# Optimization experiments

Hardware: AMD Instinct MI355X
Metric: run time of the kernel (lower is better)

Reference implementation:

```python
import jax, jax.numpy as jnp
import numpy as np

B, S, LD, Hh, Ww = 64, 32, 16, 32, 18
D, NH, HD, FF, L = 512, 8, 64, 2048, 6
IN = LD * Hh * Ww  # 9216
EPS = 1e-5


def setup_inputs() -> dict:
    key = jax.random.key(0)
    ks = jax.random.split(key, 8)
    p = lambda k, s: jax.random.normal(k, s, jnp.float32) * 0.02
    return {
        "x": jax.random.normal(ks[0], (B, S, LD, Hh, Ww), jnp.float32),
        "inp_w": p(ks[1], (D, IN)), "inp_b": jnp.zeros((D,), jnp.float32),
        "in_proj_w": p(ks[2], (L, 3 * D, D)), "in_proj_b": jnp.zeros((L, 3 * D), jnp.float32),
        "out_w": p(ks[3], (L, D, D)), "out_b": jnp.zeros((L, D), jnp.float32),
        "ln1_w": jnp.ones((L, D), jnp.float32), "ln1_b": jnp.zeros((L, D), jnp.float32),
        "ln2_w": jnp.ones((L, D), jnp.float32), "ln2_b": jnp.zeros((L, D), jnp.float32),
        "ff1_w": p(ks[4], (L, FF, D)), "ff1_b": jnp.zeros((L, FF), jnp.float32),
        "ff2_w": p(ks[5], (L, D, FF)), "ff2_b": jnp.zeros((L, D), jnp.float32),
        "outp_w": p(ks[6], (IN, D)), "outp_b": jnp.zeros((IN,), jnp.float32),
    }


def _layernorm(x, w, b):
    mu = jnp.mean(x, -1, keepdims=True)
    var = jnp.mean(jnp.square(x - mu), -1, keepdims=True)
    return (x - mu) * jax.lax.rsqrt(var + EPS) * w + b


def _rope(x, cos, sin):
    # x: [B,S,NH,HD]; torchtune interleaved-pair rotation, rope applied BEFORE qk projection
    x2 = x.reshape(*x.shape[:-1], HD // 2, 2)
    x0, x1 = x2[..., 0], x2[..., 1]
    c = cos[None, :, None, :]
    s = sin[None, :, None, :]
    out = jnp.stack([x0 * c - x1 * s, x1 * c + x0 * s], axis=-1)
    return out.reshape(x.shape)


def reference(x, inp_w, inp_b, in_proj_w, in_proj_b, out_w, out_b,
              ln1_w, ln1_b, ln2_w, ln2_b, ff1_w, ff1_b, ff2_w, ff2_b,
              outp_w, outp_b):
    b, s = x.shape[0], x.shape[1]
    h = x.reshape(b, s, IN) @ inp_w.T + inp_b  # [B,S,D]

    theta = 1.0 / (10000.0 ** (jnp.arange(0, HD, 2, dtype=jnp.float32) / HD))
    ang = jnp.arange(s, dtype=jnp.float32)[:, None] * theta  # [S, HD/2]
    cos, sin = jnp.cos(ang), jnp.sin(ang)
    mask = jnp.triu(jnp.full((s, s), -jnp.inf, jnp.float32), k=1)  # causal additive mask
    scale = 1.0 / np.sqrt(HD)

    for i in range(L):
        # RoPE on full hidden state (pre-projection), used for q and k; v uses unrotated h
        hr = _rope(h.reshape(b, s, NH, HD), cos, sin).reshape(b, s, D)
        wq, wk, wv = in_proj_w[i, :D], in_proj_w[i, D:2 * D], in_proj_w[i, 2 * D:]
        bq, bk, bv = in_proj_b[i, :D], in_proj_b[i, D:2 * D], in_proj_b[i, 2 * D:]
        q = (hr @ wq.T + bq).reshape(b, s, NH, HD)
        k = (hr @ wk.T + bk).reshape(b, s, NH, HD)
        v = (h @ wv.T + bv).reshape(b, s, NH, HD)
        scores = jnp.einsum('bqhd,bkhd->bhqk', q, k) * scale + mask
        attn = jax.nn.softmax(scores, axis=-1)
        ctx = jnp.einsum('bhqk,bkhd->bqhd', attn, v).reshape(b, s, D)
        sa = ctx @ out_w[i].T + out_b[i]
        h = _layernorm(h + sa, ln1_w[i], ln1_b[i])  # post-norm (norm_first=False)
        ff = jax.nn.gelu(h @ ff1_w[i].T + ff1_b[i], approximate=False) @ ff2_w[i].T + ff2_b[i]
        h = _layernorm(h + ff, ln2_w[i], ln2_b[i])

    out = h @ outp_w.T + outp_b
    return out.reshape(b, s, LD, Hh, Ww)
```

## Files before the change

### kernel.cpp

```cpp
#include <hip/hip_runtime.h>
#include <hip/hip_bf16.h>
#include <math.h>


typedef __attribute__((ext_vector_type(8))) short bf16x8;
typedef __attribute__((ext_vector_type(4))) short bf16x4;
typedef __attribute__((ext_vector_type(8))) float f32x8;
typedef __attribute__((ext_vector_type(4))) float f32x4;

#define LN_EPS 1e-5f

__device__ inline float bf2f(__hip_bfloat16 v) { return __bfloat162float(v); }
__device__ inline __hip_bfloat16 f2bf(float f) { return __float2bfloat16(f); }

__device__ __forceinline__ void gload_lds16(const __hip_bfloat16* g, __hip_bfloat16* l) {
    __builtin_amdgcn_global_load_lds(
        (const __attribute__((address_space(1))) unsigned*)g,
        (__attribute__((address_space(3))) unsigned*)l, 16, 0, 0);
}

__device__ __forceinline__ void sync_tile() {
    asm volatile("s_waitcnt vmcnt(0) lgkmcnt(0)" ::: "memory");
    __builtin_amdgcn_s_barrier();
    asm volatile("" ::: "memory");
}

__global__ __launch_bounds__(1024) void rope_prep(float* __restrict__ tab) {
    const int t = threadIdx.x;
    const int s = t >> 5, p = t & 31;
    const float theta = powf(10000.f, -(float)p / 32.f);
    float sn, cs;
    sincosf((float)s * theta, &sn, &cs);
    tab[t * 2] = cs;
    tab[t * 2 + 1] = sn;
}

struct CvtSeg { const float* src; __hip_bfloat16* dst; };
struct CvtArgs { CvtSeg seg[16]; long cum[17]; };

__global__ __launch_bounds__(256) void convert_all(CvtArgs a, long total8) {
    for (long i = (long)blockIdx.x * 256 + threadIdx.x; i < total8;
         i += (long)gridDim.x * 256) {
        int s = 0;
        while (i >= a.cum[s + 1]) ++s;
        const long off = i - a.cum[s];
        const f32x8 x = *((const f32x8*)a.seg[s].src + off);
        union { bf16x8 v; __hip_bfloat16 b[8]; } o;
#pragma unroll
        for (int t = 0; t < 8; ++t) o.b[t] = f2bf(x[t]);
        *((bf16x8*)a.seg[s].dst + off) = o.v;
    }
}

template<int BM, int BN, int EPI, int OUT, int AMODE, int SWZ>
__global__ __launch_bounds__(256) void gemm_bt(
    const void* __restrict__ Araw, int bn_split,
    const float* __restrict__ rtab,
    const __hip_bfloat16* __restrict__ W,
    const __hip_bfloat16* __restrict__ bias,
    void* __restrict__ Cv,
    int M, int N, int Ktot, int KC)
{
    constexpr int FM = BM / 32, FN = BN / 32;
    constexpr int CPT_A = BM / 32, CPT_B = BN / 32;
    __shared__ __align__(16) __hip_bfloat16 sA[BM * 64];
    __shared__ __align__(16) __hip_bfloat16 sB[BN * 64];

    const int tid = threadIdx.x, lane = tid & 63, wave = tid >> 6;
    const int wr = wave >> 1, wc = wave & 1;
    const int lr = lane & 15, lk = lane >> 4;

    int bm, bn, zz;
    if (SWZ == 0) {
        const int nbm = gridDim.x, nbn = gridDim.y;
        const int nwg = nbm * nbn;
        const int orig = blockIdx.y * nbm + blockIdx.x;
        const int q8 = nwg >> 3, r8 = nwg & 7;
        const int xcd = orig & 7, loc = orig >> 3;
        const int f = (xcd < r8 ? xcd * (q8 + 1) : r8 * (q8 + 1) + (xcd - r8) * q8) + loc;
        bm = f % nbm; bn = f / nbm; zz = blockIdx.z;
    } else {
        const int bid = blockIdx.x;
        const int xcd = bid & 7, loc = bid >> 3;
        const int nbn = N / BN;
        const int per = (gridDim.x >> 3) / nbn;
        bn = loc % nbn;
        const int gid = xcd * per + loc / nbn;
        bm = gid % (M / BM); zz = gid / (M / BM);
    }
    const int kbeg = zz * KC, kend = kbeg + KC;
    const bool dorot = (AMODE == 2) && (bn < bn_split);

    const __hip_bfloat16* Ab = (const __hip_bfloat16*)Araw + (long)bm * BM * Ktot;
    const float*          Af = (const float*)Araw + (long)bm * BM * Ktot;
    const __hip_bfloat16* Wb = W + (long)bn * BN * Ktot;

    f32x4 acc[FM][FN];
#pragma unroll
    for (int i = 0; i < FM; ++i)
#pragma unroll
        for (int j = 0; j < FN; ++j) acc[i][j] = (f32x4){0.f, 0.f, 0.f, 0.f};

    f32x8  aregf[CPT_A];
    bf16x8 aregb[CPT_A];
    f32x8  csreg[CPT_A];

    auto stageA_g = [&](int k0) {
#pragma unroll
        for (int c = 0; c < CPT_A; ++c) {
            const int ch = tid + c * 256, row = ch >> 3, co = ch & 7;
            gload_lds16(&Ab[(long)row * Ktot + k0 + ((co ^ (row & 7)) * 8)],
                        (__hip_bfloat16*)((char*)sA + ch * 16));
        }
    };
    auto stageB_g = [&](int k0) {
#pragma unroll
        for (int c = 0; c < CPT_B; ++c) {
            const int ch = tid + c * 256, row = ch >> 3, co = ch & 7;
            gload_lds16(&Wb[(long)row * Ktot + k0 + ((co ^ (row & 7)) * 8)],
                        (__hip_bfloat16*)((char*)sB + ch * 16));
        }
    };
    auto issueA = [&](int k0) {
#pragma unroll
        for (int c = 0; c < CPT_A; ++c) {
            const int ch = tid + c * 256, row = ch >> 3, co = ch & 7;
            if (AMODE == 1) aregf[c] = *(const f32x8*)&Af[(long)row * Ktot + k0 + co * 8];
            if (AMODE == 2) {
                aregb[c] = *(const bf16x8*)&Ab[(long)row * Ktot + k0 + co * 8];
                if (dorot)
                    csreg[c] = *(const f32x8*)&rtab[((bm * BM + row) & 31) * 64 + co * 8];
            }
        }
    };
    auto writeA = [&]() {
#pragma unroll
        for (int c = 0; c < CPT_A; ++c) {
            const int ch = tid + c * 256, row = ch >> 3, co = ch & 7;
            union { bf16x8 v; __hip_bfloat16 b[8]; } t;
            if (AMODE == 1) {
#pragma unroll
                for (int j = 0; j < 8; ++j) t.b[j] = f2bf(aregf[c][j]);
            } else {
                t.v = aregb[c];
                if (dorot) {
#pragma unroll
                    for (int qd = 0; qd < 4; ++qd) {
                        const float c_ = csreg[c][qd * 2], sn = csreg[c][qd * 2 + 1];
                        const float x0 = bf2f(t.b[2 * qd]);
                        const float x1 = bf2f(t.b[2 * qd + 1]);
                        t.b[2 * qd]     = f2bf(x0 * c_ - x1 * sn);
                        t.b[2 * qd + 1] = f2bf(x1 * c_ + x0 * sn);
                    }
                }
            }
            *(bf16x8*)((char*)sA + row * 128 + ((co ^ (row & 7)) << 4)) = t.v;
        }
    };
    auto compute = [&]() {
        bf16x8 af[2][FM], bfr[2][FN];
#pragma unroll
        for (int ks = 0; ks < 2; ++ks) {
#pragma unroll
            for (int i = 0; i < FM; ++i) {
                const int row = wr * (BM / 2) + i * 16 + lr;
                const int co = ks * 4 + lk;
                af[ks][i] = *(const bf16x8*)((const char*)sA + row * 128 +
                                             ((co ^ (row & 7)) << 4));
            }
#pragma unroll
            for (int j = 0; j < FN; ++j) {
                const int row = wc * (BN / 2) + j * 16 + lr;
                const int co = ks * 4 + lk;
                bfr[ks][j] = *(const bf16x8*)((const char*)sB + row * 128 +
                                              ((co ^ (row & 7)) << 4));
            }
        }
#pragma unroll
        for (int ks = 0; ks < 2; ++ks)
#pragma unroll
            for (int i = 0; i < FM; ++i)
#pragma unroll
                for (int j = 0; j < FN; ++j)
                    acc[i][j] = __builtin_amdgcn_mfma_f32_16x16x32_bf16(
                        af[ks][i], bfr[ks][j], acc[i][j], 0, 0, 0);
    };

    if (AMODE != 0) issueA(kbeg);
    for (int k0 = kbeg; k0 < kend; k0 += 64) {
        if (k0 > kbeg) __builtin_amdgcn_s_barrier();
        if (AMODE == 0) stageA_g(k0);
        stageB_g(k0);
        if (AMODE != 0) writeA();
        sync_tile();
        if (AMODE != 0 && k0 + 64 < kend) issueA(k0 + 64);
        compute();
    }

    const int row0 = bm * BM + wr * (BM / 2);
    const int col0 = bn * BN + wc * (BN / 2);
    if (OUT == 1) {
        float* Cp = (float*)Cv + (long)zz * M * N;
#pragma unroll
        for (int i = 0; i < FM; ++i)
#pragma unroll
            for (int j = 0; j < FN; ++j) {
                const int col = col0 + j * 16 + lr;
#pragma unroll
                for (int r = 0; r < 4; ++r)
                    Cp[(long)(row0 + i * 16 + lk * 4 + r) * N + col] = acc[i][j][r];
            }
    } else {
#pragma unroll
        for (int i = 0; i < FM; ++i)
#pragma unroll
            for (int j = 0; j < FN; ++j) {
                const int col = col0 + j * 16 + lr;
                const float bv = bf2f(bias[col]);
#pragma unroll
                for (int r = 0; r < 4; ++r) {
                    const int row = row0 + i * 16 + lk * 4 + r;
                    float v = acc[i][j][r] + bv;
                    if (EPI == 1) v = 0.5f * v * (1.0f + erff(v * 0.70710678118654752f));
                    const long idx = (long)row * N + col;
                    if (OUT == 2) ((float*)Cv)[idx] = v;
                    else          ((__hip_bfloat16*)Cv)[idx] = f2bf(v);
                }
            }
    }
}

__global__ __launch_bounds__(256) void sk_reduce_rt(
    const float* __restrict__ part, const __hip_bfloat16* __restrict__ bias,
    __hip_bfloat16* __restrict__ out, int SK)
{
    const long MN = 2048L * 512;
    const long i4 = ((long)blockIdx.x * 256 + threadIdx.x) * 4;
    f32x4 s = (f32x4){0.f, 0.f, 0.f, 0.f};
    for (int z = 0; z < SK; ++z) s += *(const f32x4*)&part[z * MN + i4];
    const int col = (int)(i4 & 511);
    union { bf16x4 v; __hip_bfloat16 b[4]; } o;
#pragma unroll
    for (int j = 0; j < 4; ++j) o.b[j] = f2bf(s[j] + bf2f(bias[col + j]));
    *(bf16x4*)&out[i4] = o.v;
}

template<int SK>
__global__ __launch_bounds__(256) void skred_add_ln(
    const float* __restrict__ part, const __hip_bfloat16* __restrict__ bias,
    const __hip_bfloat16* __restrict__ resid,
    const __hip_bfloat16* __restrict__ w, const __hip_bfloat16* __restrict__ b,
    __hip_bfloat16* __restrict__ out)
{
    const long MN = 2048L * 512;
    const int wave = threadIdx.x >> 6, lane = threadIdx.x & 63;
    const long row = (long)blockIdx.x * 4 + wave;
    const long base = row * 512 + lane * 8;

    f32x8 acc = *(const f32x8*)&part[base];
#pragma unroll
    for (int z = 1; z < SK; ++z) acc += *(const f32x8*)&part[z * MN + base];

    union { bf16x8 v; __hip_bfloat16 b[8]; } ur, uo;
    ur.v = *(const bf16x8*)&resid[base];

    float x[8];
    float s = 0.f, s2 = 0.f;
#pragma unroll
    for (int j = 0; j < 8; ++j) {
        const int col = lane * 8 + j;
        x[j] = acc[j] + bf2f(bias[col]) + bf2f(ur.b[j]);
        s += x[j];
        s2 += x[j] * x[j];
    }
#pragma unroll
    for (int off = 32; off; off >>= 1) {
        s  += __shfl_xor(s, off);
        s2 += __shfl_xor(s2, off);
    }
    const float mu = s * (1.f / 512.f);
    const float var = s2 * (1.f / 512.f) - mu * mu;
    const float rs = rsqrtf(var + LN_EPS);
#pragma unroll
    for (int j = 0; j < 8; ++j) {
        const int col = lane * 8 + j;
        uo.b[j] = f2bf((x[j] - mu) * rs * bf2f(w[col]) + bf2f(b[col]));
    }
    *(bf16x8*)&out[base] = uo.v;
}

__global__ __launch_bounds__(256) void attn_mfma(
    const __hip_bfloat16* __restrict__ qkv, __hip_bfloat16* __restrict__ ctx)
{
    __shared__ __align__(16) __hip_bfloat16 sP[4][32 * 32];
    __shared__ __align__(16) __hip_bfloat16 sVT[4][64 * 32];

    const int wave = threadIdx.x >> 6, lane = threadIdx.x & 63;
    const int bh = blockIdx.x * 4 + wave;
    const int b = bh >> 3, head = bh & 7;
    const long tok0 = (long)b * 32;
    const int lr = lane & 15, lk = lane >> 4;

    const __hip_bfloat16* Qb = qkv + tok0 * 1536 + head * 64;
    const __hip_bfloat16* Kb = Qb + 512;
    const __hip_bfloat16* Vb = Qb + 1024;

#pragma unroll
    for (int t = 0; t < 4; ++t) {
        const int c = lane + t * 64, row = c >> 3, d0 = (c & 7) * 8;
        union { bf16x8 v; __hip_bfloat16 e[8]; } u;
        u.v = *(const bf16x8*)&Vb[(long)row * 1536 + d0];
#pragma unroll
        for (int e = 0; e < 8; ++e) sVT[wave][(d0 + e) * 32 + row] = u.e[e];
    }

    f32x4 sc[2][2];
#pragma unroll
    for (int i = 0; i < 2; ++i)
#pragma unroll
        for (int j = 0; j < 2; ++j) sc[i][j] = (f32x4){0.f, 0.f, 0.f, 0.f};
#pragma unroll
    for (int ks = 0; ks < 2; ++ks) {
        bf16x8 aq[2], bk[2];
#pragma unroll
        for (int i = 0; i < 2; ++i)
            aq[i] = *(const bf16x8*)&Qb[(long)(i * 16 + lr) * 1536 + ks * 32 + lk * 8];
#pragma unroll
        for (int j = 0; j < 2; ++j)
            bk[j] = *(const bf16x8*)&Kb[(long)(j * 16 + lr) * 1536 + ks * 32 + lk * 8];
#pragma unroll
        for (int i = 0; i < 2; ++i)
#pragma unroll
            for (int j = 0; j < 2; ++j)
                sc[i][j] = __builtin_amdgcn_mfma_f32_16x16x32_bf16(aq[i], bk[j], sc[i][j], 0, 0, 0);
    }

    float p[2][2][4], inv[2][4];
#pragma unroll
    for (int i = 0; i < 2; ++i) {
#pragma unroll
        for (int r = 0; r < 4; ++r) {
            const int row = i * 16 + lk * 4 + r;
            float m = -3.0e38f;
#pragma unroll
            for (int j = 0; j < 2; ++j) {
                const int col = j * 16 + lr;
                const float v = (col <= row) ? sc[i][j][r] * 0.125f : -3.0e38f;
                p[i][j][r] = v;
                m = fmaxf(m, v);
            }
#pragma unroll
            for (int off = 1; off < 16; off <<= 1)
                m = fmaxf(m, __shfl_xor(m, off));
            float l = 0.f;
#pragma unroll
            for (int j = 0; j < 2; ++j) {
                p[i][j][r] = expf(p[i][j][r] - m);
                l += p[i][j][r];
            }
#pragma unroll
            for (int off = 1; off < 16; off <<= 1)
                l += __shfl_xor(l, off);
            inv[i][r] = 1.f / l;
        }
    }

#pragma unroll
    for (int i = 0; i < 2; ++i)
#pragma unroll
        for (int j = 0; j < 2; ++j)
#pragma unroll
            for (int r = 0; r < 4; ++r)
                sP[wave][(i * 16 + lk * 4 + r) * 32 + j * 16 + lr] = f2bf(p[i][j][r]);

    bf16x8 pa[2], vb[4];
#pragma unroll
    for (int i = 0; i < 2; ++i)
        pa[i] = *(const bf16x8*)&sP[wave][(i * 16 + lr) * 32 + lk * 8];
#pragma unroll
    for (int j = 0; j < 4; ++j)
        vb[j] = *(const bf16x8*)&sVT[wave][(j * 16 + lr) * 32 + lk * 8];

    f32x4 o[2][4];
#pragma unroll
    for (int i = 0; i < 2; ++i)
#pragma unroll
        for (int j = 0; j < 4; ++j) {
            o[i][j] = (f32x4){0.f, 0.f, 0.f, 0.f};
            o[i][j] = __builtin_amdgcn_mfma_f32_16x16x32_bf16(pa[i], vb[j], o[i][j], 0, 0, 0);
        }

#pragma unroll
    for (int i = 0; i < 2; ++i)
#pragma unroll
        for (int j = 0; j < 4; ++j) {
            const int col = j * 16 + lr;
#pragma unroll
            for (int r = 0; r < 4; ++r) {
                const int row = i * 16 + lk * 4 + r;
                ctx[(tok0 + row) * 512 + head * 64 + col] = f2bf(o[i][j][r] * inv[i][r]);
            }
        }
}

extern "C" void kernel_launch(void* const* d_in, const int* in_sizes, int n_in,
                              void* d_out, int out_size, void* d_ws, size_t ws_size,
                              hipStream_t stream)
{
    const int M = 2048;
    __hip_bfloat16* wts = (__hip_bfloat16*)d_ws;

    const long O_INPW   = 0;
    const long O_INPROJ = 4718592;
    const long O_OUTW   = 9437184;
    const long O_FF1    = 11010048;
    const long O_FF2    = 17301504;
    const long O_OUTPW  = 23592960;
    const long O_INPB   = 28311552;
    const long O_INPROJB= 28312064;
    const long O_OUTB   = 28321280;
    const long O_LN1W   = 28324352;
    const long O_LN1B   = 28327424;
    const long O_LN2W   = 28330496;
    const long O_LN2B   = 28333568;
    const long O_FF1B   = 28336640;
    const long O_FF2B   = 28348928;
    const long O_OUTPB  = 28352000;
    const long O_ACT    = 28361216;

    __hip_bfloat16* h   = wts + O_ACT;
    __hip_bfloat16* ht  = h   + (long)M * 512;
    __hip_bfloat16* qkv = ht  + (long)M * 512;
    __hip_bfloat16* ctx = qkv + (long)M * 1536;
    __hip_bfloat16* ffh = ctx + (long)M * 512;
    float* rtab = (float*)(ffh + (long)M * 2048);
    float* skpart = (float*)((__hip_bfloat16*)rtab + 4096);

    const long skpart_byte_off = (char*)skpart - (char*)d_ws;
    const int zin = (ws_size >= (size_t)skpart_byte_off + 16L * M * 512 * 4) ? 16 : 8;

    rope_prep<<<1, 1024, 0, stream>>>(rtab);

    const int  cidx[16] = {1, 3, 5, 11, 13, 15, 2, 4, 6, 7, 8, 9, 10, 12, 14, 16};
    const long coff[16] = {O_INPW, O_INPROJ, O_OUTW, O_FF1, O_FF2, O_OUTPW,
                           O_INPB, O_INPROJB, O_OUTB, O_LN1W, O_LN1B, O_LN2W,
                           O_LN2B, O_FF1B, O_FF2B, O_OUTPB};
    const long csz[16]  = {4718592, 4718592, 1572864, 6291456, 6291456, 4718592,
                           512, 9216, 3072, 3072, 3072, 3072, 3072, 12288, 3072, 9216};
    CvtArgs ca;
    long cum = 0;
    for (int s = 0; s < 16; ++s) {
        ca.seg[s].src = (const float*)d_in[cidx[s]];
        ca.seg[s].dst = wts + coff[s];
        ca.cum[s] = cum;
        cum += csz[s] / 8;
    }
    ca.cum[16] = cum;
    convert_all<<<2048, 256, 0, stream>>>(ca, cum);

    gemm_bt<128, 128, 0, 1, 1, 1><<<64 * zin, 256, 0, stream>>>(
        d_in[0], 0, rtab, wts + O_INPW, wts + O_INPB, skpart, M, 512, 9216, 9216 / zin);
    sk_reduce_rt<<<1024, 256, 0, stream>>>(skpart, wts + O_INPB, h, zin);

    for (int i = 0; i < 6; ++i) {
        const __hip_bfloat16* wqkv = wts + O_INPROJ + (long)i * 1536 * 512;
        const __hip_bfloat16* bqkv = wts + O_INPROJB + i * 1536;

        gemm_bt<64, 64, 0, 0, 2, 0><<<dim3(32, 24), 256, 0, stream>>>(
            h, 16, rtab, wqkv, bqkv, qkv, M, 1536, 512, 512);
        attn_mfma<<<128, 256, 0, stream>>>(qkv, ctx);
        gemm_bt<64, 64, 0, 1, 0, 0><<<dim3(32, 8, 2), 256, 0, stream>>>(
            ctx, 0, rtab, wts + O_OUTW + (long)i * 512 * 512, wts + O_OUTB + i * 512,
            skpart, M, 512, 512, 256);
        skred_add_ln<2><<<512, 256, 0, stream>>>(
            skpart, wts + O_OUTB + i * 512, h,
            wts + O_LN1W + i * 512, wts + O_LN1B + i * 512, ht);
        gemm_bt<64, 64, 1, 0, 0, 0><<<dim3(32, 32), 256, 0, stream>>>(
            ht, 0, rtab, wts + O_FF1 + (long)i * 2048 * 512, wts + O_FF1B + i * 2048,
            ffh, M, 2048, 512, 512);
        gemm_bt<64, 64, 0, 1, 0, 0><<<dim3(32, 8, 4), 256, 0, stream>>>(
            ffh, 0, rtab, wts + O_FF2 + (long)i * 512 * 2048, wts + O_FF2B + i * 512,
            skpart, M, 512, 2048, 512);
        skred_add_ln<4><<<512, 256, 0, stream>>>(
            skpart, wts + O_FF2B + i * 512, ht,
            wts + O_LN2W + i * 512, wts + O_LN2B + i * 512, h);
    }

    gemm_bt<128, 128, 0, 2, 0, 0><<<dim3(16, 72), 256, 0, stream>>>(
        h, 0, rtab, wts + O_OUTPW, wts + O_OUTPB, d_out, M, 9216, 512, 512);
}
```

Measured before the change: 524.9 us.

## Double-buffer LDS in GEMM kernels and fix input split-K at eight

Adds a PIPE template option that double-buffers the shared-memory A/B tiles, so loads for the next K tile are issued before computing on the current one and one barrier per iteration is removed. It is enabled for the QKV, FF1 and FF2 GEMMs. Separately, the input projection now always uses split-K of 8 instead of picking 16 when workspace allows, and the reduction is templated on SK with an unrolled loop. Double buffering doubles LDS use per block and may lower occupancy. The fixed split changes parallelism for the large-K input GEMM.

```diff
diff --git a/kernel.cpp b/kernel.cpp
--- a/kernel.cpp
+++ b/kernel.cpp
@@ -52,7 +52,7 @@
     }
 }
 
-template<int BM, int BN, int EPI, int OUT, int AMODE, int SWZ>
+template<int BM, int BN, int EPI, int OUT, int AMODE, int SWZ, int PIPE>
 __global__ __launch_bounds__(256) void gemm_bt(
     const void* __restrict__ Araw, int bn_split,
     const float* __restrict__ rtab,
@@ -63,8 +63,9 @@
 {
     constexpr int FM = BM / 32, FN = BN / 32;
     constexpr int CPT_A = BM / 32, CPT_B = BN / 32;
-    __shared__ __align__(16) __hip_bfloat16 sA[BM * 64];
-    __shared__ __align__(16) __hip_bfloat16 sB[BN * 64];
+    constexpr int NBUF = PIPE ? 2 : 1;
+    __shared__ __align__(16) __hip_bfloat16 sA[NBUF][BM * 64];
+    __shared__ __align__(16) __hip_bfloat16 sB[NBUF][BN * 64];
 
     const int tid = threadIdx.x, lane = tid & 63, wave = tid >> 6;
     const int wr = wave >> 1, wc = wave & 1;
@@ -105,20 +106,20 @@
     bf16x8 aregb[CPT_A];
     f32x8  csreg[CPT_A];
 
-    auto stageA_g = [&](int k0) {
+    auto stageA_g = [&](int buf, int k0) {
 #pragma unroll
         for (int c = 0; c < CPT_A; ++c) {
             const int ch = tid + c * 256, row = ch >> 3, co = ch & 7;
             gload_lds16(&Ab[(long)row * Ktot + k0 + ((co ^ (row & 7)) * 8)],
-                        (__hip_bfloat16*)((char*)sA + ch * 16));
+                        (__hip_bfloat16*)((char*)&sA[buf][0] + ch * 16));
         }
     };
-    auto stageB_g = [&](int k0) {
+    auto stageB_g = [&](int buf, int k0) {
 #pragma unroll
         for (int c = 0; c < CPT_B; ++c) {
             const int ch = tid + c * 256, row = ch >> 3, co = ch & 7;
             gload_lds16(&Wb[(long)row * Ktot + k0 + ((co ^ (row & 7)) * 8)],
-                        (__hip_bfloat16*)((char*)sB + ch * 16));
+                        (__hip_bfloat16*)((char*)&sB[buf][0] + ch * 16));
         }
     };
     auto issueA = [&](int k0) {
@@ -133,7 +134,7 @@
             }
         }
     };
-    auto writeA = [&]() {
+    auto writeA = [&](int buf) {
 #pragma unroll
         for (int c = 0; c < CPT_A; ++c) {
             const int ch = tid + c * 256, row = ch >> 3, co = ch & 7;
@@ -154,10 +155,10 @@
                     }
                 }
             }
-            *(bf16x8*)((char*)sA + row * 128 + ((co ^ (row & 7)) << 4)) = t.v;
+            *(bf16x8*)((char*)&sA[buf][0] + row * 128 + ((co ^ (row & 7)) << 4)) = t.v;
         }
     };
-    auto compute = [&]() {
+    auto compute = [&](int buf) {
         bf16x8 af[2][FM], bfr[2][FN];
 #pragma unroll
         for (int ks = 0; ks < 2; ++ks) {
@@ -165,14 +166,14 @@
             for (int i = 0; i < FM; ++i) {
                 const int row = wr * (BM / 2) + i * 16 + lr;
                 const int co = ks * 4 + lk;
-                af[ks][i] = *(const bf16x8*)((const char*)sA + row * 128 +
+                af[ks][i] = *(const bf16x8*)((const char*)&sA[buf][0] + row * 128 +
                                              ((co ^ (row & 7)) << 4));
             }
 #pragma unroll
             for (int j = 0; j < FN; ++j) {
                 const int row = wc * (BN / 2) + j * 16 + lr;
                 const int co = ks * 4 + lk;
-                bfr[ks][j] = *(const bf16x8*)((const char*)sB + row * 128 +
+                bfr[ks][j] = *(const bf16x8*)((const char*)&sB[buf][0] + row * 128 +
                                               ((co ^ (row & 7)) << 4));
             }
         }
@@ -186,15 +187,36 @@
                         af[ks][i], bfr[ks][j], acc[i][j], 0, 0, 0);
     };
 
-    if (AMODE != 0) issueA(kbeg);
-    for (int k0 = kbeg; k0 < kend; k0 += 64) {
-        if (k0 > kbeg) __builtin_amdgcn_s_barrier();
-        if (AMODE == 0) stageA_g(k0);
-        stageB_g(k0);
-        if (AMODE != 0) writeA();
+    if (PIPE == 0) {
+        if (AMODE != 0) issueA(kbeg);
+        for (int k0 = kbeg; k0 < kend; k0 += 64) {
+            if (k0 > kbeg) __builtin_amdgcn_s_barrier();
+            if (AMODE == 0) stageA_g(0, k0);
+            stageB_g(0, k0);
+            if (AMODE != 0) writeA(0);
+            sync_tile();
+            if (AMODE != 0 && k0 + 64 < kend) issueA(k0 + 64);
+            compute(0);
+        }
+    } else {
+        if (AMODE == 0) stageA_g(0, kbeg); else issueA(kbeg);
+        stageB_g(0, kbeg);
+        if (AMODE != 0) writeA(0);
         sync_tile();
-        if (AMODE != 0 && k0 + 64 < kend) issueA(k0 + 64);
-        compute();
+        int cur = 0;
+        for (int k0 = kbeg; k0 < kend; k0 += 64) {
+            const bool hn = (k0 + 64 < kend);
+            if (hn) {
+                if (AMODE == 0) stageA_g(cur ^ 1, k0 + 64); else issueA(k0 + 64);
+                stageB_g(cur ^ 1, k0 + 64);
+            }
+            compute(cur);
+            if (hn) {
+                if (AMODE != 0) writeA(cur ^ 1);
+                sync_tile();
+            }
+            cur ^= 1;
+        }
     }
 
     const int row0 = bm * BM + wr * (BM / 2);
@@ -230,13 +252,15 @@
     }
 }
 
-__global__ __launch_bounds__(256) void sk_reduce_rt(
+template<int SK>
+__global__ __launch_bounds__(256) void sk_reduce(
     const float* __restrict__ part, const __hip_bfloat16* __restrict__ bias,
-    __hip_bfloat16* __restrict__ out, int SK)
+    __hip_bfloat16* __restrict__ out)
 {
     const long MN = 2048L * 512;
     const long i4 = ((long)blockIdx.x * 256 + threadIdx.x) * 4;
     f32x4 s = (f32x4){0.f, 0.f, 0.f, 0.f};
+#pragma unroll
     for (int z = 0; z < SK; ++z) s += *(const f32x4*)&part[z * MN + i4];
     const int col = (int)(i4 & 511);
     union { bf16x4 v; __hip_bfloat16 b[4]; } o;
@@ -436,9 +460,6 @@
     float* rtab = (float*)(ffh + (long)M * 2048);
     float* skpart = (float*)((__hip_bfloat16*)rtab + 4096);
 
-    const long skpart_byte_off = (char*)skpart - (char*)d_ws;
-    const int zin = (ws_size >= (size_t)skpart_byte_off + 16L * M * 512 * 4) ? 16 : 8;
-
     rope_prep<<<1, 1024, 0, stream>>>(rtab);
 
     const int  cidx[16] = {1, 3, 5, 11, 13, 15, 2, 4, 6, 7, 8, 9, 10, 12, 14, 16};
@@ -458,27 +479,27 @@
     ca.cum[16] = cum;
     convert_all<<<2048, 256, 0, stream>>>(ca, cum);
 
-    gemm_bt<128, 128, 0, 1, 1, 1><<<64 * zin, 256, 0, stream>>>(
-        d_in[0], 0, rtab, wts + O_INPW, wts + O_INPB, skpart, M, 512, 9216, 9216 / zin);
-    sk_reduce_rt<<<1024, 256, 0, stream>>>(skpart, wts + O_INPB, h, zin);
+    gemm_bt<128, 128, 0, 1, 1, 1, 0><<<512, 256, 0, stream>>>(
+        d_in[0], 0, rtab, wts + O_INPW, wts + O_INPB, skpart, M, 512, 9216, 1152);
+    sk_reduce<8><<<1024, 256, 0, stream>>>(skpart, wts + O_INPB, h);
 
     for (int i = 0; i < 6; ++i) {
         const __hip_bfloat16* wqkv = wts + O_INPROJ + (long)i * 1536 * 512;
         const __hip_bfloat16* bqkv = wts + O_INPROJB + i * 1536;
 
-        gemm_bt<64, 64, 0, 0, 2, 0><<<dim3(32, 24), 256, 0, stream>>>(
+        gemm_bt<64, 64, 0, 0, 2, 0, 1><<<dim3(32, 24), 256, 0, stream>>>(
             h, 16, rtab, wqkv, bqkv, qkv, M, 1536, 512, 512);
         attn_mfma<<<128, 256, 0, stream>>>(qkv, ctx);
-        gemm_bt<64, 64, 0, 1, 0, 0><<<dim3(32, 8, 2), 256, 0, stream>>>(
+        gemm_bt<64, 64, 0, 1, 0, 0, 0><<<dim3(32, 8, 2), 256, 0, stream>>>(
             ctx, 0, rtab, wts + O_OUTW + (long)i * 512 * 512, wts + O_OUTB + i * 512,
             skpart, M, 512, 512, 256);
         skred_add_ln<2><<<512, 256, 0, stream>>>(
             skpart, wts + O_OUTB + i * 512, h,
             wts + O_LN1W + i * 512, wts + O_LN1B + i * 512, ht);
-        gemm_bt<64, 64, 1, 0, 0, 0><<<dim3(32, 32), 256, 0, stream>>>(
+        gemm_bt<64, 64, 1, 0, 0, 0, 1><<<dim3(32, 32), 256, 0, stream>>>(
             ht, 0, rtab, wts + O_FF1 + (long)i * 2048 * 512, wts + O_FF1B + i * 2048,
             ffh, M, 2048, 512, 512);
-        gemm_bt<64, 64, 0, 1, 0, 0><<<dim3(32, 8, 4), 256, 0, stream>>>(
+        gemm_bt<64, 64, 0, 1, 0, 0, 1><<<dim3(32, 8, 4), 256, 0, stream>>>(
             ffh, 0, rtab, wts + O_FF2 + (long)i * 512 * 2048, wts + O_FF2B + i * 512,
             skpart, M, 512, 2048, 512);
         skred_add_ln<4><<<512, 256, 0, stream>>>(
@@ -486,6 +507,6 @@
             wts + O_LN2W + i * 512, wts + O_LN2B + i * 512, h);
     }
 
-    gemm_bt<128, 128, 0, 2, 0, 0><<<dim3(16, 72), 256, 0, stream>>>(
+    gemm_bt<128, 128, 0, 2, 0, 0, 0><<<dim3(16, 72), 256, 0, stream>>>(
         h, 0, rtab, wts + O_OUTPW, wts + O_OUTPB, d_out, M, 9216, 512, 512);
 }
```

Result: faster. 507.2 us (-3.4%).
